# Optimization experiments

Measured on AMD Instinct MI355X. Metric: run time of the kernel, lower is better.

Reference implementation:

```python
import jax, jax.numpy as jnp
import numpy as np

LN_EPS = 1e-5  # ParlAI LAYER_NORM_EPS
B, S, D, H, E, V = 4, 512, 512, 2048, 8, 32000


def setup_inputs() -> dict:
    key = jax.random.key(0)
    ks = jax.random.split(key, 6)
    x = jax.random.normal(ks[0], (B, S, D), dtype=jnp.float32)
    orig_input = jax.random.randint(ks[1], (B, S), 0, V)          # token ids
    hash_bin_map = jax.random.randint(ks[2], (V,), 0, E, dtype=jnp.int32)
    W1 = jax.random.normal(ks[3], (E, D, H), dtype=jnp.float32) * 0.02
    b1 = jnp.zeros((E, H), dtype=jnp.float32)
    W2 = jax.random.normal(ks[4], (E, H, D), dtype=jnp.float32) * 0.02
    b2 = jnp.zeros((E, D), dtype=jnp.float32)
    gamma = jnp.ones((D,), dtype=jnp.float32)
    beta = jnp.zeros((D,), dtype=jnp.float32)
    return {"x": x, "W1": W1, "b1": b1, "W2": W2, "b2": b2,
            "gamma": gamma, "beta": beta,
            "orig_input": orig_input, "hash_bin_map": hash_bin_map}


def _layernorm(z, gamma, beta):
    mu = jnp.mean(z, axis=-1, keepdims=True)
    var = jnp.var(z, axis=-1, keepdims=True)
    return (z - mu) * jax.lax.rsqrt(var + LN_EPS) * gamma + beta


def reference(x, W1, b1, W2, b2, gamma, beta, orig_input, hash_bin_map):
    # per-token expert assignment via hash of token id
    bins = hash_bin_map[orig_input]                    # [B, S] int
    n_experts = W1.shape[0]
    ffn_out = jnp.zeros_like(x)
    # loop over the small fixed expert set; mask-combine replaces gather/scatter
    for e in range(n_experts):
        h = jax.nn.relu(jnp.einsum('bsd,dh->bsh', x, W1[e]) + b1[e])
        y = jnp.einsum('bsh,hd->bsd', h, W2[e]) + b2[e]
        ffn_out = ffn_out + jnp.where((bins == e)[..., None], y, 0.0)
    # residual + shared LayerNorm (every token belongs to exactly one bin)
    return _layernorm(x + ffn_out, gamma, beta)
```

## Files before the change

kernel.cpp:

```cpp
#include <hip/hip_runtime.h>
#include <hip/hip_bf16.h>
#include <stdint.h>

#define D_DIM 512
#define H_DIM 2048
#define E_NUM 8
#define TM 64
#define CAP 2560
#define MAXRT 6

typedef __attribute__((ext_vector_type(8))) short short8;
typedef __attribute__((ext_vector_type(4))) float floatx4;

union Pack4 { short4 u; __hip_bfloat16 h[4]; };

__global__ __launch_bounds__(256) void bin_kernel(
    const int* __restrict__ orig, const int* __restrict__ hmap,
    int* __restrict__ gidx, int* __restrict__ meta, int ntok)
{
    __shared__ int cnt[E_NUM];
    __shared__ int cur[E_NUM];
    int tid = threadIdx.x;
    if (tid < E_NUM) cnt[tid] = 0;
    __syncthreads();
    for (int t = tid; t < ntok; t += 256) {
        int b = hmap[orig[t]];
        atomicAdd(&cnt[b], 1);
    }
    __syncthreads();
    if (tid == 0) {
        int off = 0;
        for (int e = 0; e < E_NUM; e++) {
            int ne = cnt[e];
            int nt = (ne + TM - 1) / TM;
            meta[e] = off; meta[8 + e] = ne; meta[16 + e] = nt;
            cur[e] = off;
            off += nt * TM;
        }
        meta[24] = off;
    }
    __syncthreads();
    for (int t = tid; t < ntok; t += 256) {
        int b = hmap[orig[t]];
        int p = atomicAdd(&cur[b], 1);
        gidx[p] = t;
    }
}

__global__ __launch_bounds__(128) void gather_kernel(
    const float* __restrict__ x, const int* __restrict__ gidx,
    const int* __restrict__ meta, __hip_bfloat16* __restrict__ Xg)
{
    int g = blockIdx.x;
    int e = -1, local = 0;
#pragma unroll
    for (int i = 0; i < E_NUM; i++) {
        int p = meta[i], nt = meta[16 + i];
        if (g >= p && g < p + nt * TM) { e = i; local = g - p; }
    }
    if (e < 0) return;
    int tid = threadIdx.x;
    __hip_bfloat16* orow = Xg + (size_t)g * D_DIM + tid * 4;
    if (local < meta[8 + e]) {
        int t = gidx[g];
        float4 v = ((const float4*)(x + (size_t)t * D_DIM))[tid];
        orow[0] = __float2bfloat16(v.x);
        orow[1] = __float2bfloat16(v.y);
        orow[2] = __float2bfloat16(v.z);
        orow[3] = __float2bfloat16(v.w);
    } else {
        orow[0] = __float2bfloat16(0.f);
        orow[1] = __float2bfloat16(0.f);
        orow[2] = __float2bfloat16(0.f);
        orow[3] = __float2bfloat16(0.f);
    }
}

template <int WN, int ASTRIDE, int KTOT, int KS, bool RELU>
__global__ __launch_bounds__(256) void moe_gemm_kernel(
    const __hip_bfloat16* __restrict__ A,
    const float* __restrict__ W,
    const float* __restrict__ bias,
    __hip_bfloat16* __restrict__ OutBf,
    __hip_bfloat16* __restrict__ OutP,
    const int* __restrict__ meta)
{
    constexpr int KLEN = KTOT / KS;
    constexpr int NI = KLEN / 64;
    constexpr int AJ = MAXRT * 64 * 8 / 256;
    const int e = blockIdx.z;
    const int n0 = blockIdx.x * 64;
    const int ks = blockIdx.y;
    const int kbase = ks * KLEN;

    int nt = meta[16 + e];
    if (nt > MAXRT) nt = MAXRT;
    const int row0 = meta[e];
    const int rows8 = nt * 64 * 8;

    __shared__ __align__(16) __hip_bfloat16 As[384 * 64];
    __shared__ __align__(16) __hip_bfloat16 Bs[64 * 64];

    const int tid = threadIdx.x;
    const int lane = tid & 63, w = tid >> 6;
    const int quad = lane >> 4, l16 = lane & 15;
    const int wr = w >> 1, wc = w & 1;
    const int kq = tid >> 4;
    const int nb = tid & 15;

    const __hip_bfloat16* Ab = A + (size_t)row0 * ASTRIDE + kbase;
    const float* Wb = W + ((size_t)e * KTOT + kbase) * WN + n0;

    floatx4 acc[MAXRT][2][2] = {};
    short8 ar[AJ];
    float4 br[4];

#define LOADA(k0) do {                                                        \
    _Pragma("unroll")                                                         \
    for (int j = 0; j < AJ; j++) {                                            \
        int c = tid + j * 256;                                                \
        if (c < rows8) {                                                      \
            int row = c >> 3;                                                 \
            int kk = ((c & 7) * 16) ^ ((row & 7) * 16);            \
            ar[j] = *(const short8*)(Ab + (size_t)row * ASTRIDE + (k0) + (kk >> 1)); \
        }                                                                     \
    }                                                                         \
} while (0)

#define WRITEA() do {                                                         \
    _Pragma("unroll")                                                         \
    for (int j = 0; j < AJ; j++) {                                            \
        int c = tid + j * 256;                                                \
        if (c < rows8)                                                        \
            *(short8*)((char*)As + c * 16) = ar[j];                           \
    }                                                                         \
} while (0)

#define LOADB(k0) do {                                                        \
    _Pragma("unroll")                                                         \
    for (int r = 0; r < 4; r++)                                               \
        br[r] = *(const float4*)(Wb + (size_t)((k0) + kq * 4 + r) * WN + nb * 4); \
} while (0)

#define WRITEB() do {                                                         \
    _Pragma("unroll")                                                         \
    for (int j = 0; j < 4; j++) {                                             \
        int n = nb * 4 + j;                                                   \
        Pack4 pk;                                                             \
        _Pragma("unroll")                                                     \
        for (int r = 0; r < 4; r++)                                           \
            pk.h[r] = __float2bfloat16(reinterpret_cast<const float*>(&br[r])[j]); \
        *(short4*)((char*)Bs + n * 128 + ((kq * 8) ^ (((n >> 2) & 7) * 16))) = pk.u; \
    }                                                                         \
} while (0)

    LOADA(0);
    LOADB(0);

    for (int i = 0; i < NI; i++) {
        __syncthreads();
        WRITEA();
        WRITEB();
        __syncthreads();
        if (i + 1 < NI) {
            LOADA((i + 1) * 64);
            LOADB((i + 1) * 64);
        }
#pragma unroll
        for (int kf = 0; kf < 2; kf++) {
            int kb = kf * 64 + quad * 16;
            short8 b[2];
#pragma unroll
            for (int ni = 0; ni < 2; ni++) {
                int n = wc * 32 + ni * 16 + l16;
                b[ni] = *(const short8*)((char*)Bs + n * 128 + (kb ^ (((n >> 2) & 7) * 16)));
            }
#pragma unroll
            for (int rt = 0; rt < MAXRT; rt++) {
                if (rt < nt) {
                    short8 a[2];
#pragma unroll
                    for (int mi = 0; mi < 2; mi++) {
                        int row = rt * 64 + wr * 32 + mi * 16 + l16;
                        a[mi] = *(const short8*)((char*)As + row * 128 + (kb ^ ((row & 7) * 16)));
                    }
#pragma unroll
                    for (int mi = 0; mi < 2; mi++)
#pragma unroll
                        for (int ni = 0; ni < 2; ni++)
                            acc[rt][mi][ni] = __builtin_amdgcn_mfma_f32_16x16x32_bf16(
                                a[mi], b[ni], acc[rt][mi][ni], 0, 0, 0);
                }
            }
        }
    }

#pragma unroll
    for (int rt = 0; rt < MAXRT; rt++) {
        if (rt >= nt) break;
#pragma unroll
        for (int ni = 0; ni < 2; ni++) {
            int col = n0 + wc * 32 + ni * 16 + l16;
            float bv = RELU ? bias[e * WN + col] : 0.f;
#pragma unroll
            for (int mi = 0; mi < 2; mi++) {
#pragma unroll
                for (int r = 0; r < 4; r++) {
                    int grow = row0 + rt * 64 + wr * 32 + mi * 16 + quad * 4 + r;
                    float v = acc[rt][mi][ni][r] + bv;
                    if constexpr (RELU) {
                        v = v > 0.f ? v : 0.f;
                        OutBf[(size_t)grow * WN + col] = __float2bfloat16(v);
                    } else {
                        OutP[((size_t)ks * CAP + grow) * WN + col] = __float2bfloat16(v);
                    }
                }
            }
        }
    }
#undef LOADA
#undef WRITEA
#undef LOADB
#undef WRITEB
}

__global__ __launch_bounds__(128) void ln_kernel(
    const float* __restrict__ x, const __hip_bfloat16* __restrict__ Yp,
    const float* __restrict__ b2,
    const float* __restrict__ gamma, const float* __restrict__ beta,
    const int* __restrict__ gidx, const int* __restrict__ meta,
    float* __restrict__ out)
{
    int g = blockIdx.x;
    int e = -1;
#pragma unroll
    for (int i = 0; i < E_NUM; i++) {
        int p = meta[i], ne = meta[8 + i];
        if (g >= p && g - p < ne) e = i;
    }
    if (e < 0) return;
    int t = gidx[g];
    int tid = threadIdx.x;

    float4 xv = ((const float4*)(x + (size_t)t * D_DIM))[tid];
    float4 bb = ((const float4*)(b2 + (size_t)e * D_DIM))[tid];
    float z0 = xv.x + bb.x, z1 = xv.y + bb.y, z2 = xv.z + bb.z, z3 = xv.w + bb.w;
#pragma unroll
    for (int s4 = 0; s4 < 4; s4++) {
        union { short4 u; __hip_bfloat16 h[4]; } yv;
        yv.u = ((const short4*)(Yp + (size_t)(s4 * CAP + g) * D_DIM))[tid];
        z0 += __bfloat162float(yv.h[0]);
        z1 += __bfloat162float(yv.h[1]);
        z2 += __bfloat162float(yv.h[2]);
        z3 += __bfloat162float(yv.h[3]);
    }

    float s = z0 + z1 + z2 + z3;
    float ss = z0 * z0 + z1 * z1 + z2 * z2 + z3 * z3;
#pragma unroll
    for (int off = 32; off > 0; off >>= 1) {
        s  += __shfl_down(s, off, 64);
        ss += __shfl_down(ss, off, 64);
    }
    __shared__ float red[4];
    int lane = tid & 63, wv = tid >> 6;
    if (lane == 0) { red[wv] = s; red[2 + wv] = ss; }
    __syncthreads();
    float S = red[0] + red[1];
    float SS = red[2] + red[3];
    float mu = S * (1.f / D_DIM);
    float var = SS * (1.f / D_DIM) - mu * mu;
    float inv = rsqrtf(var + 1e-5f);

    float4 gv = ((const float4*)gamma)[tid];
    float4 bv = ((const float4*)beta)[tid];
    float4 o;
    o.x = (z0 - mu) * inv * gv.x + bv.x;
    o.y = (z1 - mu) * inv * gv.y + bv.y;
    o.z = (z2 - mu) * inv * gv.z + bv.z;
    o.w = (z3 - mu) * inv * gv.w + bv.w;
    ((float4*)(out + (size_t)t * D_DIM))[tid] = o;
}

extern "C" void kernel_launch(void* const* d_in, const int* in_sizes, int n_in,
                              void* d_out, int out_size, void* d_ws, size_t ws_size,
                              hipStream_t stream)
{
    const float* x     = (const float*)d_in[0];
    const float* W1    = (const float*)d_in[1];
    const float* b1    = (const float*)d_in[2];
    const float* W2    = (const float*)d_in[3];
    const float* b2    = (const float*)d_in[4];
    const float* gamma = (const float*)d_in[5];
    const float* beta  = (const float*)d_in[6];
    const int* orig    = (const int*)d_in[7];
    const int* hmap    = (const int*)d_in[8];
    float* out = (float*)d_out;
    int ntok = in_sizes[7];

    char* ws = (char*)d_ws;
    __hip_bfloat16* Yp  = (__hip_bfloat16*)(ws);
    __hip_bfloat16* Hb  = (__hip_bfloat16*)(ws + 10485760);
    __hip_bfloat16* Xg  = (__hip_bfloat16*)(ws + 20971520);
    int*            gidx= (int*)(ws + 23592960);
    int*            meta= (int*)(ws + 23603200);

    hipLaunchKernelGGL(bin_kernel, dim3(1), dim3(256), 0, stream,
                       orig, hmap, gidx, meta, ntok);
    hipLaunchKernelGGL(gather_kernel, dim3(CAP), dim3(128), 0, stream,
                       x, gidx, meta, Xg);
    hipLaunchKernelGGL((moe_gemm_kernel<H_DIM, D_DIM, D_DIM, 1, true>),
                       dim3(H_DIM / 64, 1, E_NUM), dim3(256), 0, stream,
                       Xg, W1, b1, Hb, (__hip_bfloat16*)nullptr, meta);
    hipLaunchKernelGGL((moe_gemm_kernel<D_DIM, H_DIM, H_DIM, 4, false>),
                       dim3(D_DIM / 64, 4, E_NUM), dim3(256), 0, stream,
                       Hb, W2, (const float*)nullptr, (__hip_bfloat16*)nullptr, Yp, meta);
    hipLaunchKernelGGL(ln_kernel, dim3(CAP), dim3(128), 0, stream,
                       x, Yp, b2, gamma, beta, gidx, meta, out);
}
```

Measured before the change: 152.9 us.

## Fuse token gather and bf16 conversion into first MoE GEMM A-loads

Removes the separate gather kernel and the bf16 Xg staging buffer. The first GEMM now reads fp32 activation rows through token indices and converts them to bf16 while writing shared memory. Padding rows are marked -1 in gidx and load as zeros. This saves a launch and a write-then-read of the gathered matrix. In exchange, the A-tile loads are now indirect, twice as wide (fp32), and each of the 32 N-blocks converts them again.

```diff
diff --git a/kernel.cpp b/kernel.cpp
--- a/kernel.cpp
+++ b/kernel.cpp
@@ -13,6 +13,7 @@
 typedef __attribute__((ext_vector_type(4))) float floatx4;
 
 union Pack4 { short4 u; __hip_bfloat16 h[4]; };
+union Pack8 { short8 s; __hip_bfloat16 h[8]; };
 
 __global__ __launch_bounds__(256) void bin_kernel(
     const int* __restrict__ orig, const int* __restrict__ hmap,
@@ -40,6 +41,8 @@
         meta[24] = off;
     }
     __syncthreads();
+    for (int g = tid; g < CAP; g += 256) gidx[g] = -1;
+    __syncthreads();
     for (int t = tid; t < ntok; t += 256) {
         int b = hmap[orig[t]];
         int p = atomicAdd(&cur[b], 1);
@@ -47,38 +50,11 @@
     }
 }
 
-__global__ __launch_bounds__(128) void gather_kernel(
-    const float* __restrict__ x, const int* __restrict__ gidx,
-    const int* __restrict__ meta, __hip_bfloat16* __restrict__ Xg)
-{
-    int g = blockIdx.x;
-    int e = -1, local = 0;
-#pragma unroll
-    for (int i = 0; i < E_NUM; i++) {
-        int p = meta[i], nt = meta[16 + i];
-        if (g >= p && g < p + nt * TM) { e = i; local = g - p; }
-    }
-    if (e < 0) return;
-    int tid = threadIdx.x;
-    __hip_bfloat16* orow = Xg + (size_t)g * D_DIM + tid * 4;
-    if (local < meta[8 + e]) {
-        int t = gidx[g];
-        float4 v = ((const float4*)(x + (size_t)t * D_DIM))[tid];
-        orow[0] = __float2bfloat16(v.x);
-        orow[1] = __float2bfloat16(v.y);
-        orow[2] = __float2bfloat16(v.z);
-        orow[3] = __float2bfloat16(v.w);
-    } else {
-        orow[0] = __float2bfloat16(0.f);
-        orow[1] = __float2bfloat16(0.f);
-        orow[2] = __float2bfloat16(0.f);
-        orow[3] = __float2bfloat16(0.f);
-    }
-}
-
-template <int WN, int ASTRIDE, int KTOT, int KS, bool RELU>
+template <int WN, int ASTRIDE, int KTOT, int KS, bool RELU, bool IND>
 __global__ __launch_bounds__(256) void moe_gemm_kernel(
     const __hip_bfloat16* __restrict__ A,
+    const float* __restrict__ Xf,
+    const int* __restrict__ gidx,
     const float* __restrict__ W,
     const float* __restrict__ bias,
     __hip_bfloat16* __restrict__ OutBf,
@@ -112,27 +88,74 @@
     const float* Wb = W + ((size_t)e * KTOT + kbase) * WN + n0;
 
     floatx4 acc[MAXRT][2][2] = {};
-    short8 ar[AJ];
+    short8 ar[IND ? 1 : AJ];
+    float4 arf[IND ? AJ : 1][2];
+    const float* tp[IND ? AJ : 1];
+    int koff[IND ? AJ : 1];
     float4 br[4];
 
+    if constexpr (IND) {
+#pragma unroll
+        for (int j = 0; j < AJ; j++) {
+            int c = tid + j * 256;
+            int row = c >> 3;
+            int kk = ((c & 7) * 16) ^ ((row & 7) * 16);
+            koff[j] = kk >> 1;
+            tp[j] = nullptr;
+            if (c < rows8) {
+                int tr = gidx[row0 + row];
+                if (tr >= 0) tp[j] = Xf + (size_t)tr * D_DIM + kbase;
+            }
+        }
+    }
+
 #define LOADA(k0) do {                                                        \
-    _Pragma("unroll")                                                         \
-    for (int j = 0; j < AJ; j++) {                                            \
-        int c = tid + j * 256;                                                \
-        if (c < rows8) {                                                      \
-            int row = c >> 3;                                                 \
-            int kk = ((c & 7) * 16) ^ ((row & 7) * 16);            \
-            ar[j] = *(const short8*)(Ab + (size_t)row * ASTRIDE + (k0) + (kk >> 1)); \
+    if constexpr (IND) {                                                      \
+        _Pragma("unroll")                                                     \
+        for (int j = 0; j < AJ; j++) {                                        \
+            if (tp[j]) {                                                      \
+                arf[j][0] = *(const float4*)(tp[j] + (k0) + koff[j]);         \
+                arf[j][1] = *(const float4*)(tp[j] + (k0) + koff[j] + 4);     \
+            } else {                                                          \
+                arf[j][0] = float4{0.f, 0.f, 0.f, 0.f};                       \
+                arf[j][1] = float4{0.f, 0.f, 0.f, 0.f};                       \
+            }                                                                 \
+        }                                                                     \
+    } else {                                                                  \
+        _Pragma("unroll")                                                     \
+        for (int j = 0; j < AJ; j++) {                                        \
+            int c = tid + j * 256;                                            \
+            if (c < rows8) {                                                  \
+                int row = c >> 3;                                             \
+                int kk = ((c & 7) * 16) ^ ((row & 7) * 16);                   \
+                ar[j] = *(const short8*)(Ab + (size_t)row * ASTRIDE + (k0) + (kk >> 1)); \
+            }                                                                 \
         }                                                                     \
     }                                                                         \
 } while (0)
 
 #define WRITEA() do {                                                         \
-    _Pragma("unroll")                                                         \
-    for (int j = 0; j < AJ; j++) {                                            \
-        int c = tid + j * 256;                                                \
-        if (c < rows8)                                                        \
-            *(short8*)((char*)As + c * 16) = ar[j];                           \
+    if constexpr (IND) {                                                      \
+        _Pragma("unroll")                                                     \
+        for (int j = 0; j < AJ; j++) {                                        \
+            int c = tid + j * 256;                                            \
+            if (c < rows8) {                                                  \
+                Pack8 pk;                                                     \
+                _Pragma("unroll")                                             \
+                for (int r = 0; r < 4; r++) {                                 \
+                    pk.h[r] = __float2bfloat16(reinterpret_cast<const float*>(&arf[j][0])[r]); \
+                    pk.h[4 + r] = __float2bfloat16(reinterpret_cast<const float*>(&arf[j][1])[r]); \
+                }                                                             \
+                *(short8*)((char*)As + c * 16) = pk.s;                        \
+            }                                                                 \
+        }                                                                     \
+    } else {                                                                  \
+        _Pragma("unroll")                                                     \
+        for (int j = 0; j < AJ; j++) {                                        \
+            int c = tid + j * 256;                                            \
+            if (c < rows8)                                                    \
+                *(short8*)((char*)As + c * 16) = ar[j];                       \
+        }                                                                     \
     }                                                                         \
 } while (0)
 
@@ -301,20 +324,19 @@
     char* ws = (char*)d_ws;
     __hip_bfloat16* Yp  = (__hip_bfloat16*)(ws);
     __hip_bfloat16* Hb  = (__hip_bfloat16*)(ws + 10485760);
-    __hip_bfloat16* Xg  = (__hip_bfloat16*)(ws + 20971520);
-    int*            gidx= (int*)(ws + 23592960);
-    int*            meta= (int*)(ws + 23603200);
+    int*            gidx= (int*)(ws + 20971520);
+    int*            meta= (int*)(ws + 20981760);
 
     hipLaunchKernelGGL(bin_kernel, dim3(1), dim3(256), 0, stream,
                        orig, hmap, gidx, meta, ntok);
-    hipLaunchKernelGGL(gather_kernel, dim3(CAP), dim3(128), 0, stream,
-                       x, gidx, meta, Xg);
-    hipLaunchKernelGGL((moe_gemm_kernel<H_DIM, D_DIM, D_DIM, 1, true>),
+    hipLaunchKernelGGL((moe_gemm_kernel<H_DIM, D_DIM, D_DIM, 1, true, true>),
                        dim3(H_DIM / 64, 1, E_NUM), dim3(256), 0, stream,
-                       Xg, W1, b1, Hb, (__hip_bfloat16*)nullptr, meta);
-    hipLaunchKernelGGL((moe_gemm_kernel<D_DIM, H_DIM, H_DIM, 4, false>),
+                       (const __hip_bfloat16*)nullptr, x, gidx, W1, b1,
+                       Hb, (__hip_bfloat16*)nullptr, meta);
+    hipLaunchKernelGGL((moe_gemm_kernel<D_DIM, H_DIM, H_DIM, 4, false, false>),
                        dim3(D_DIM / 64, 4, E_NUM), dim3(256), 0, stream,
-                       Hb, W2, (const float*)nullptr, (__hip_bfloat16*)nullptr, Yp, meta);
+                       Hb, (const float*)nullptr, (const int*)nullptr, W2,
+                       (const float*)nullptr, (__hip_bfloat16*)nullptr, Yp, meta);
     hipLaunchKernelGGL(ln_kernel, dim3(CAP), dim3(128), 0, stream,
                        x, Yp, b2, gamma, beta, gidx, meta, out);
 }
```

After: 162.9 us. 6.6% more time.
